# Performance work log

Measured on AMD Instinct MI355X. Metric: run time of the kernel, lower is better.

The kernel has to match this reference:

```python
import jax, jax.numpy as jnp
import numpy as np

EMBED_DIM = 768
NUM_HEADS = 12
HEAD_DIM = EMBED_DIM // NUM_HEADS


def setup_inputs() -> dict:
    key = jax.random.key(0)
    k1, k2, k3, k4 = jax.random.split(key, 4)
    B, N, D = 8, 1024, EMBED_DIM
    x = jax.random.normal(k1, (B, N, D), dtype=jnp.float32)
    # qkv Linear (no bias): torch weight [3D, D]; we store transposed [D, 3D]
    W_qkv = jax.random.normal(k2, (D, 3 * D), dtype=jnp.float32) * (D ** -0.5)
    # projection Linear with bias
    W_proj = jax.random.normal(k3, (D, D), dtype=jnp.float32) * (D ** -0.5)
    b_proj = jax.random.normal(k4, (D,), dtype=jnp.float32) * 0.01
    return {"x": x, "W_qkv": W_qkv, "W_proj": W_proj, "b_proj": b_proj}


def reference(x, W_qkv, W_proj, b_proj):
    B, N, D = x.shape
    h, d = NUM_HEADS, HEAD_DIM
    scaling = d ** -0.5
    qkv = x @ W_qkv  # [B, N, 3D]
    # 'b n (qkv h d) -> qkv b h n d'
    qkv = qkv.reshape(B, N, 3, h, d).transpose(2, 0, 3, 1, 4)
    q, k, v = qkv[0], qkv[1], qkv[2]  # each [B, h, N, d]
    energy = jnp.einsum('bhid,bhjd->bhij', q, k) * scaling  # [B, h, N, N]
    att = jax.nn.softmax(energy, axis=-1)
    out = jnp.einsum('bhij,bhjd->bhid', att, v)  # [B, h, N, d]
    out = out.transpose(0, 2, 1, 3).reshape(B, N, D)  # 'b h n d -> b n (h d)'
    out = out @ W_proj + b_proj
    return out
```

## Files before the change

kernel.cpp:

```cpp
#include <hip/hip_runtime.h>
#include <hip/hip_bf16.h>

#define NUM_B 8
#define SEQ   1024
#define DIM   768
#define NH    12
#define HD    64

typedef __bf16 bf16x8 __attribute__((ext_vector_type(8)));
typedef float  f32x4  __attribute__((ext_vector_type(4)));
typedef unsigned int u32;

#define QSCL 0.18033688011112042f
#define SM_SHIFT 8.0f

__device__ __forceinline__ unsigned short f2bf(float f) {
  unsigned int u = __float_as_uint(f);
  u += 0x7FFFu + ((u >> 16) & 1u);
  return (unsigned short)(u >> 16);
}

__device__ __forceinline__ float fexp2(float x) { return __builtin_exp2f(x); }

__device__ __forceinline__ void gload_lds16(const void* g, void* l) {
  __builtin_amdgcn_global_load_lds(
      (const __attribute__((address_space(1))) unsigned int*)g,
      (__attribute__((address_space(3))) unsigned int*)l, 16, 0, 0);
}

__global__ void cvt_kernel(const float* __restrict__ in, unsigned short* __restrict__ out, int n) {
  int i = (blockIdx.x * blockDim.x + threadIdx.x) * 4;
  if (i >= n) return;
  float4 v = *(const float4*)(in + i);
  ushort4 o = { f2bf(v.x), f2bf(v.y), f2bf(v.z), f2bf(v.w) };
  *(ushort4*)(out + i) = o;
}

__global__ void tcvt_kernel(const float* __restrict__ in, unsigned short* __restrict__ out,
                            int R, int C) {
  __shared__ unsigned short tile[32][33];
  int c0 = blockIdx.x * 32, r0 = blockIdx.y * 32;
  int tx = threadIdx.x, ty = threadIdx.y;
  #pragma unroll
  for (int i = 0; i < 32; i += 8)
    tile[ty + i][tx] = f2bf(in[(size_t)(r0 + ty + i) * C + c0 + tx]);
  __syncthreads();
  #pragma unroll
  for (int i = 0; i < 32; i += 8)
    out[(size_t)(c0 + ty + i) * R + r0 + tx] = tile[tx][ty + i];
}

template<bool QKV>
__global__ __launch_bounds__(256) void gemm_bf16(
    const unsigned short* __restrict__ A,
    const unsigned short* __restrict__ Bt,
    int K,
    unsigned short* __restrict__ qb,
    unsigned short* __restrict__ kb,
    unsigned short* __restrict__ vt,
    float* __restrict__ outp,
    const float* __restrict__ bias)
{
  __shared__ short As[2][128 * 32];
  __shared__ short Bs[2][128 * 32];
  const int m0 = blockIdx.x * 128, n0 = blockIdx.y * 128;
  const int t = threadIdx.x;
  const int lane = t & 63, w = t >> 6;
  const int l15 = lane & 15, g = lane >> 4;
  const int wm = w >> 1, wn = w & 1;
  const int sx = (l15 >> 1) & 3;

  const int ch0 = t, ch1 = t + 256;
  const size_t szK = (size_t)K;
  const int r0c = ch0 >> 2, g0c = (ch0 & 3) ^ ((ch0 >> 3) & 3);
  const int r1c = ch1 >> 2, g1c = (ch1 & 3) ^ ((ch1 >> 3) & 3);
  const unsigned short* Ag0 = A  + (size_t)(m0 + r0c) * szK + g0c * 8;
  const unsigned short* Ag1 = A  + (size_t)(m0 + r1c) * szK + g1c * 8;
  const unsigned short* Bg0 = Bt + (size_t)(n0 + r0c) * szK + g0c * 8;
  const unsigned short* Bg1 = Bt + (size_t)(n0 + r1c) * szK + g1c * 8;
  const int lb0 = w * 512, lb1 = 2048 + w * 512;

  f32x4 zv = {0.f, 0.f, 0.f, 0.f};
  f32x4 acc[4][4];
  #pragma unroll
  for (int i = 0; i < 4; ++i)
    #pragma unroll
    for (int j = 0; j < 4; ++j) acc[i][j] = zv;

  gload_lds16(Ag0, &As[0][lb0]);
  gload_lds16(Ag1, &As[0][lb1]);
  gload_lds16(Bg0, &Bs[0][lb0]);
  gload_lds16(Bg1, &Bs[0][lb1]);
  asm volatile("s_waitcnt vmcnt(0)" ::: "memory");
  __syncthreads();

  int cur = 0;
  for (int k0 = 0; k0 < K; k0 += 32) {
    if (k0 + 32 < K) {
      gload_lds16(Ag0 + k0 + 32, &As[cur ^ 1][lb0]);
      gload_lds16(Ag1 + k0 + 32, &As[cur ^ 1][lb1]);
      gload_lds16(Bg0 + k0 + 32, &Bs[cur ^ 1][lb0]);
      gload_lds16(Bg1 + k0 + 32, &Bs[cur ^ 1][lb1]);
    }
    bf16x8 af[4], bfr[4];
    #pragma unroll
    for (int i = 0; i < 4; ++i)
      af[i]  = *(const bf16x8*)&As[cur][(wm*64 + i*16 + l15) * 32 + ((g ^ sx) << 3)];
    #pragma unroll
    for (int i = 0; i < 4; ++i)
      bfr[i] = *(const bf16x8*)&Bs[cur][(wn*64 + i*16 + l15) * 32 + ((g ^ sx) << 3)];
    #pragma unroll
    for (int i = 0; i < 4; ++i)
      #pragma unroll
      for (int j = 0; j < 4; ++j)
        acc[i][j] = __builtin_amdgcn_mfma_f32_16x16x32_bf16(af[i], bfr[j], acc[i][j], 0, 0, 0);
    asm volatile("s_waitcnt vmcnt(0)" ::: "memory");
    __syncthreads();
    cur ^= 1;
  }

  const int mbase = m0 + wm * 64, nbase = n0 + wn * 64;
  if (QKV) {
    #pragma unroll
    for (int i = 0; i < 4; ++i) {
      #pragma unroll
      for (int j = 0; j < 4; ++j) {
        int n = nbase + j * 16 + l15;
        int which = n / DIM;
        int jr = n - which * DIM;
        int head = jr >> 6, dd = jr & 63;
        float sc = (which == 0) ? QSCL : 1.0f;
        #pragma unroll
        for (int r = 0; r < 4; ++r) {
          int m = mbase + i * 16 + g * 4 + r;
          int bb = m >> 10, nn = m & 1023;
          unsigned short val = f2bf(acc[i][j][r] * sc);
          size_t bh = (size_t)bb * NH + head;
          if (which == 0)      qb[(bh * SEQ + nn) * HD + dd] = val;
          else if (which == 1) kb[(bh * SEQ + nn) * HD + dd] = val;
          else {
            int nnp = (nn & ~31) | ((nn & 12) << 1) | ((nn & 16) >> 2) | (nn & 3);
            vt[(bh * HD + dd) * SEQ + nnp] = val;
          }
        }
      }
    }
  } else {
    #pragma unroll
    for (int i = 0; i < 4; ++i)
      #pragma unroll
      for (int j = 0; j < 4; ++j) {
        int n = nbase + j * 16 + l15;
        float bv = bias[n];
        #pragma unroll
        for (int r = 0; r < 4; ++r) {
          int m = mbase + i * 16 + g * 4 + r;
          outp[(size_t)m * DIM + n] = acc[i][j][r] + bv;
        }
      }
  }
}

__global__ __launch_bounds__(256) void attn_kernel(
    const unsigned short* __restrict__ qb,
    const unsigned short* __restrict__ kb,
    const unsigned short* __restrict__ vt,
    unsigned short* __restrict__ ao)
{
  __shared__ short lds[2][2][4096];
  const int bid = blockIdx.x;
  const int qt = (bid & 7) * 128;
  const int bh = bid >> 3;
  const int t = threadIdx.x, lane = t & 63, w = t >> 6;
  const int l15 = lane & 15, g = lane >> 4;
  const unsigned short* Qp = qb + (size_t)bh * SEQ * HD;
  const unsigned short* Kp = kb + (size_t)bh * SEQ * HD;
  const unsigned short* Vp = vt + (size_t)bh * HD * SEQ;
  const int q0 = qt + w * 32;
  const int swz = l15 & 7;

  int offK[2], offV[2], ldso[2];
  #pragma unroll
  for (int i = 0; i < 2; ++i) {
    int chunk = ((w * 2 + i) << 6) + lane;
    int row = chunk >> 3;
    int c = (chunk & 7) ^ (row & 7);
    offK[i] = row * HD + c * 8;
    offV[i] = row * SEQ + c * 8;
    ldso[i] = (w * 2 + i) << 9;
  }

  bf16x8 bq[2][2];
  #pragma unroll
  for (int nq = 0; nq < 2; ++nq)
    #pragma unroll
    for (int kk = 0; kk < 2; ++kk)
      bq[nq][kk] = *(const bf16x8*)(Qp + (size_t)(q0 + nq*16 + l15) * HD + kk*32 + g*8);

  bf16x8 ones;
  #pragma unroll
  for (int i = 0; i < 8; ++i) ones[i] = (__bf16)1.0f;

  f32x4 zv = {0.f, 0.f, 0.f, 0.f};
  f32x4 sinit = { -SM_SHIFT, -SM_SHIFT, -SM_SHIFT, -SM_SHIFT };
  f32x4 accO[2][4];
  f32x4 rsac[2] = { zv, zv };
  #pragma unroll
  for (int nq = 0; nq < 2; ++nq)
    #pragma unroll
    for (int fn = 0; fn < 4; ++fn) accO[nq][fn] = zv;

  #pragma unroll
  for (int i = 0; i < 2; ++i) {
    gload_lds16(Kp + offK[i], &lds[0][0][ldso[i]]);
    gload_lds16(Vp + offV[i], &lds[0][1][ldso[i]]);
  }
  asm volatile("s_waitcnt vmcnt(0)" ::: "memory");
  __syncthreads();

  int cur = 0;
  for (int kt = 0; kt < SEQ; kt += 64) {
    if (kt + 64 < SEQ) {
      #pragma unroll
      for (int i = 0; i < 2; ++i) {
        gload_lds16(Kp + (size_t)(kt + 64) * HD + offK[i], &lds[cur ^ 1][0][ldso[i]]);
        gload_lds16(Vp + (kt + 64) + offV[i], &lds[cur ^ 1][1][ldso[i]]);
      }
    }
    const short* Kb = &lds[cur][0][0];
    const short* Vb = &lds[cur][1][0];

    f32x4 s[2][4];
    #pragma unroll
    for (int nq = 0; nq < 2; ++nq)
      #pragma unroll
      for (int fm = 0; fm < 4; ++fm) s[nq][fm] = sinit;
    #pragma unroll
    for (int fm = 0; fm < 4; ++fm)
      #pragma unroll
      for (int kk = 0; kk < 2; ++kk) {
        bf16x8 ak = *(const bf16x8*)&Kb[(fm*16 + l15) * 64 + (((kk*4 + g) ^ swz) << 3)];
        s[0][fm] = __builtin_amdgcn_mfma_f32_16x16x32_bf16(ak, bq[0][kk], s[0][fm], 0, 0, 0);
        s[1][fm] = __builtin_amdgcn_mfma_f32_16x16x32_bf16(ak, bq[1][kk], s[1][fm], 0, 0, 0);
      }

    bf16x8 av[4][2];
    #pragma unroll
    for (int fn = 0; fn < 4; ++fn)
      #pragma unroll
      for (int cc = 0; cc < 2; ++cc)
        av[fn][cc] = *(const bf16x8*)&Vb[(fn*16 + l15) * 64 + (((cc*4 + g) ^ swz) << 3)];

    bf16x8 pb[2][2];
    #pragma unroll
    for (int nq = 0; nq < 2; ++nq) {
      #pragma unroll
      for (int cc = 0; cc < 2; ++cc)
        #pragma unroll
        for (int h = 0; h < 2; ++h)
          #pragma unroll
          for (int r = 0; r < 4; ++r)
            pb[nq][cc][h*4 + r] = (__bf16)fexp2(s[nq][2*cc + h][r]);
      rsac[nq] = __builtin_amdgcn_mfma_f32_16x16x32_bf16(ones, pb[nq][0], rsac[nq], 0, 0, 0);
      rsac[nq] = __builtin_amdgcn_mfma_f32_16x16x32_bf16(ones, pb[nq][1], rsac[nq], 0, 0, 0);
    }

    #pragma unroll
    for (int cc = 0; cc < 2; ++cc)
      #pragma unroll
      for (int fn = 0; fn < 4; ++fn) {
        accO[0][fn] = __builtin_amdgcn_mfma_f32_16x16x32_bf16(av[fn][cc], pb[0][cc], accO[0][fn], 0, 0, 0);
        accO[1][fn] = __builtin_amdgcn_mfma_f32_16x16x32_bf16(av[fn][cc], pb[1][cc], accO[1][fn], 0, 0, 0);
      }

    asm volatile("s_waitcnt vmcnt(0)" ::: "memory");
    __syncthreads();
    cur ^= 1;
  }

  const int bb = bh / NH, hh = bh - bb * NH;
  #pragma unroll
  for (int nq = 0; nq < 2; ++nq) {
    float inv = 1.0f / rsac[nq][0];
    int q = q0 + nq * 16 + l15;
    unsigned short* op = ao + ((size_t)(bb * SEQ + q)) * DIM + hh * HD + g * 4;
    #pragma unroll
    for (int fn = 0; fn < 4; ++fn) {
      ushort4 o = { f2bf(accO[nq][fn][0] * inv), f2bf(accO[nq][fn][1] * inv),
                    f2bf(accO[nq][fn][2] * inv), f2bf(accO[nq][fn][3] * inv) };
      *(ushort4*)(op + fn * 16) = o;
    }
  }
}

extern "C" void kernel_launch(void* const* d_in, const int* in_sizes, int n_in,
                              void* d_out, int out_size, void* d_ws, size_t ws_size,
                              hipStream_t stream) {
  const float* x     = (const float*)d_in[0];
  const float* Wqkv  = (const float*)d_in[1];
  const float* Wproj = (const float*)d_in[2];
  const float* bproj = (const float*)d_in[3];
  float* out = (float*)d_out;

  unsigned short* ws = (unsigned short*)d_ws;
  const size_t NX = (size_t)NUM_B * SEQ * DIM;
  unsigned short* x_bf    = ws;
  unsigned short* Wqkv_t  = x_bf + NX;
  unsigned short* Wproj_t = Wqkv_t + (size_t)3 * DIM * DIM;
  unsigned short* qbuf    = Wproj_t + (size_t)DIM * DIM;
  unsigned short* kbuf    = qbuf + NX;
  unsigned short* vtb     = kbuf + NX;
  unsigned short* attb    = vtb + NX;

  cvt_kernel<<<dim3((unsigned)(NX / 4 / 256)), 256, 0, stream>>>(x, x_bf, (int)NX);
  tcvt_kernel<<<dim3(3 * DIM / 32, DIM / 32), dim3(32, 8), 0, stream>>>(Wqkv, Wqkv_t, DIM, 3 * DIM);
  tcvt_kernel<<<dim3(DIM / 32, DIM / 32), dim3(32, 8), 0, stream>>>(Wproj, Wproj_t, DIM, DIM);

  gemm_bf16<true><<<dim3(64, 18), 256, 0, stream>>>(
      x_bf, Wqkv_t, DIM, qbuf, kbuf, vtb, nullptr, nullptr);

  attn_kernel<<<dim3(NUM_B * NH * (SEQ / 128)), 256, 0, stream>>>(qbuf, kbuf, vtb, attb);

  gemm_bf16<false><<<dim3(64, 6), 256, 0, stream>>>(
      attb, Wproj_t, DIM, nullptr, nullptr, nullptr, out, bproj);
}
```

Baseline: 205.5 us.

## Triple-buffer LDS tiles with partial vmcnt waits in GEMM and attention

Both the GEMM and attention kernels move from double-buffered to triple-buffered LDS staging, issuing loads three tiles ahead. Each iteration waits only for the oldest tile with a partial vmcnt count instead of draining all outstanding loads, which keeps more global-to-LDS traffic in flight behind the MFMA work. This uses more shared memory per block, which may reduce occupancy, and it relies on the vmcnt counts matching exactly four loads per tile.

```diff
diff --git a/kernel.cpp b/kernel.cpp
--- a/kernel.cpp
+++ b/kernel.cpp
@@ -26,6 +26,12 @@
   __builtin_amdgcn_global_load_lds(
       (const __attribute__((address_space(1))) unsigned int*)g,
       (__attribute__((address_space(3))) unsigned int*)l, 16, 0, 0);
+}
+
+__device__ __forceinline__ void wait_tiles(int rem) {
+  if (rem >= 2)      asm volatile("s_waitcnt vmcnt(8)" ::: "memory");
+  else if (rem == 1) asm volatile("s_waitcnt vmcnt(4)" ::: "memory");
+  else               asm volatile("s_waitcnt vmcnt(0)" ::: "memory");
 }
 
 __global__ void cvt_kernel(const float* __restrict__ in, unsigned short* __restrict__ out, int n) {
@@ -61,8 +67,8 @@
     float* __restrict__ outp,
     const float* __restrict__ bias)
 {
-  __shared__ short As[2][128 * 32];
-  __shared__ short Bs[2][128 * 32];
+  __shared__ short As[3][128 * 32];
+  __shared__ short Bs[3][128 * 32];
   const int m0 = blockIdx.x * 128, n0 = blockIdx.y * 128;
   const int t = threadIdx.x;
   const int lane = t & 63, w = t >> 6;
@@ -87,36 +93,42 @@
     #pragma unroll
     for (int j = 0; j < 4; ++j) acc[i][j] = zv;
 
-  gload_lds16(Ag0, &As[0][lb0]);
-  gload_lds16(Ag1, &As[0][lb1]);
-  gload_lds16(Bg0, &Bs[0][lb0]);
-  gload_lds16(Bg1, &Bs[0][lb1]);
-  asm volatile("s_waitcnt vmcnt(0)" ::: "memory");
-  __syncthreads();
-
-  int cur = 0;
-  for (int k0 = 0; k0 < K; k0 += 32) {
-    if (k0 + 32 < K) {
-      gload_lds16(Ag0 + k0 + 32, &As[cur ^ 1][lb0]);
-      gload_lds16(Ag1 + k0 + 32, &As[cur ^ 1][lb1]);
-      gload_lds16(Bg0 + k0 + 32, &Bs[cur ^ 1][lb0]);
-      gload_lds16(Bg1 + k0 + 32, &Bs[cur ^ 1][lb1]);
-    }
+  const int NT = K / 32;
+
+  #pragma unroll
+  for (int p = 0; p < 3; ++p) {
+    gload_lds16(Ag0 + p * 32, &As[p][lb0]);
+    gload_lds16(Ag1 + p * 32, &As[p][lb1]);
+    gload_lds16(Bg0 + p * 32, &Bs[p][lb0]);
+    gload_lds16(Bg1 + p * 32, &Bs[p][lb1]);
+  }
+
+  for (int ti = 0; ti < NT; ++ti) {
+    wait_tiles(NT - 1 - ti);
+    __builtin_amdgcn_s_barrier();
+    __builtin_amdgcn_sched_barrier(0);
+    const int b = ti % 3;
     bf16x8 af[4], bfr[4];
     #pragma unroll
     for (int i = 0; i < 4; ++i)
-      af[i]  = *(const bf16x8*)&As[cur][(wm*64 + i*16 + l15) * 32 + ((g ^ sx) << 3)];
+      af[i]  = *(const bf16x8*)&As[b][(wm*64 + i*16 + l15) * 32 + ((g ^ sx) << 3)];
     #pragma unroll
     for (int i = 0; i < 4; ++i)
-      bfr[i] = *(const bf16x8*)&Bs[cur][(wn*64 + i*16 + l15) * 32 + ((g ^ sx) << 3)];
+      bfr[i] = *(const bf16x8*)&Bs[b][(wn*64 + i*16 + l15) * 32 + ((g ^ sx) << 3)];
     #pragma unroll
     for (int i = 0; i < 4; ++i)
       #pragma unroll
       for (int j = 0; j < 4; ++j)
         acc[i][j] = __builtin_amdgcn_mfma_f32_16x16x32_bf16(af[i], bfr[j], acc[i][j], 0, 0, 0);
-    asm volatile("s_waitcnt vmcnt(0)" ::: "memory");
-    __syncthreads();
-    cur ^= 1;
+    __builtin_amdgcn_sched_barrier(0);
+    __builtin_amdgcn_s_barrier();
+    if (ti + 3 < NT) {
+      const int k3 = (ti + 3) * 32;
+      gload_lds16(Ag0 + k3, &As[b][lb0]);
+      gload_lds16(Ag1 + k3, &As[b][lb1]);
+      gload_lds16(Bg0 + k3, &Bs[b][lb0]);
+      gload_lds16(Bg1 + k3, &Bs[b][lb1]);
+    }
   }
 
   const int mbase = m0 + wm * 64, nbase = n0 + wn * 64;
@@ -167,7 +179,7 @@
     const unsigned short* __restrict__ vt,
     unsigned short* __restrict__ ao)
 {
-  __shared__ short lds[2][2][4096];
+  __shared__ short lds[3][2][4096];
   const int bid = blockIdx.x;
   const int qt = (bid & 7) * 128;
   const int bh = bid >> 3;
@@ -210,25 +222,23 @@
     #pragma unroll
     for (int fn = 0; fn < 4; ++fn) accO[nq][fn] = zv;
 
-  #pragma unroll
-  for (int i = 0; i < 2; ++i) {
-    gload_lds16(Kp + offK[i], &lds[0][0][ldso[i]]);
-    gload_lds16(Vp + offV[i], &lds[0][1][ldso[i]]);
-  }
-  asm volatile("s_waitcnt vmcnt(0)" ::: "memory");
-  __syncthreads();
-
-  int cur = 0;
-  for (int kt = 0; kt < SEQ; kt += 64) {
-    if (kt + 64 < SEQ) {
-      #pragma unroll
-      for (int i = 0; i < 2; ++i) {
-        gload_lds16(Kp + (size_t)(kt + 64) * HD + offK[i], &lds[cur ^ 1][0][ldso[i]]);
-        gload_lds16(Vp + (kt + 64) + offV[i], &lds[cur ^ 1][1][ldso[i]]);
-      }
-    }
-    const short* Kb = &lds[cur][0][0];
-    const short* Vb = &lds[cur][1][0];
+  const int NT = SEQ / 64;
+
+  #pragma unroll
+  for (int p = 0; p < 3; ++p)
+    #pragma unroll
+    for (int i = 0; i < 2; ++i) {
+      gload_lds16(Kp + (size_t)(p * 64) * HD + offK[i], &lds[p][0][ldso[i]]);
+      gload_lds16(Vp + (p * 64) + offV[i], &lds[p][1][ldso[i]]);
+    }
+
+  for (int ti = 0; ti < NT; ++ti) {
+    wait_tiles(NT - 1 - ti);
+    __builtin_amdgcn_s_barrier();
+    __builtin_amdgcn_sched_barrier(0);
+    const int b = ti % 3;
+    const short* Kb = &lds[b][0][0];
+    const short* Vb = &lds[b][1][0];
 
     f32x4 s[2][4];
     #pragma unroll
@@ -273,9 +283,16 @@
         accO[1][fn] = __builtin_amdgcn_mfma_f32_16x16x32_bf16(av[fn][cc], pb[1][cc], accO[1][fn], 0, 0, 0);
       }
 
-    asm volatile("s_waitcnt vmcnt(0)" ::: "memory");
-    __syncthreads();
-    cur ^= 1;
+    __builtin_amdgcn_sched_barrier(0);
+    __builtin_amdgcn_s_barrier();
+    if (ti + 3 < NT) {
+      const int kt3 = (ti + 3) * 64;
+      #pragma unroll
+      for (int i = 0; i < 2; ++i) {
+        gload_lds16(Kp + (size_t)kt3 * HD + offK[i], &lds[b][0][ldso[i]]);
+        gload_lds16(Vp + kt3 + offV[i], &lds[b][1][ldso[i]]);
+      }
+    }
   }
 
   const int bb = bh / NH, hh = bh - bb * NH;
```

Result: slower. 218.2 us (+6.2%).
